# Optimization experiments

Hardware: AMD Instinct MI355X
Metric: run time of the kernel (lower is better)

The kernel has to match this reference:

```python
import jax, jax.numpy as jnp
import numpy as np

B, N, E = 4096, 64, 256      # graph pairs, nodes per drug, directed edges per drug
F, H, FP = 128, 64, 2048     # node feat dim, hidden dim, fingerprint dim


def setup_inputs() -> dict:
    key = jax.random.key(0)
    ks = jax.random.split(key, 14)
    return {
        "x1": jax.random.normal(ks[0], (B, N, F), jnp.float32),
        "x2": jax.random.normal(ks[1], (B, N, F), jnp.float32),
        "edge1": jax.random.randint(ks[2], (B, 2, E), 0, N, jnp.int32),
        "edge2": jax.random.randint(ks[3], (B, 2, E), 0, N, jnp.int32),
        "fp1": jax.random.uniform(ks[4], (B, FP), jnp.float32),
        "fp2": jax.random.uniform(ks[5], (B, FP), jnp.float32),
        "W1": jax.random.normal(ks[6], (F, H), jnp.float32) * 0.05,
        "b1": jnp.zeros((H,), jnp.float32),
        "W2": jax.random.normal(ks[7], (H, H), jnp.float32) * 0.05,
        "b2": jnp.zeros((H,), jnp.float32),
        "Wm1": jax.random.normal(ks[8], (2 * H + 2 * FP, 256), jnp.float32) * 0.02,
        "bm1": jnp.zeros((256,), jnp.float32),
        "Wm2": jax.random.normal(ks[9], (256, 1), jnp.float32) * 0.05,
        "bm2": jnp.zeros((1,), jnp.float32),
    }


def gcn_conv(x, src, dst, W, b):
    """PyG GCNConv: self-loops + symmetric normalization, aggregated at dst."""
    n = x.shape[0]
    loops = jnp.arange(n, dtype=src.dtype)
    s = jnp.concatenate([src, loops])
    d = jnp.concatenate([dst, loops])
    deg = jax.ops.segment_sum(jnp.ones_like(d, jnp.float32), d, num_segments=n)
    norm = jax.lax.rsqrt(deg)                      # deg >= 1 due to self-loops
    xw = x @ W                                     # [n, H]
    msg = xw[s] * (norm[s] * norm[d])[:, None]     # [n+E, H]
    return jax.ops.segment_sum(msg, d, num_segments=n) + b


def encode(x, edges, W1, b1, W2, b2):
    src, dst = edges[0], edges[1]
    h = jax.nn.relu(gcn_conv(x, src, dst, W1, b1))
    h = jax.nn.relu(gcn_conv(h, src, dst, W2, b2))
    return h.mean(axis=0)                          # global_mean_pool (1 graph)


_encode_b = jax.vmap(encode, in_axes=(0, 0, None, None, None, None))


def reference(x1, x2, edge1, edge2, fp1, fp2, W1, b1, W2, b2, Wm1, bm1, Wm2, bm2):
    h1 = _encode_b(x1, edge1, W1, b1, W2, b2)      # [B, H]
    h2 = _encode_b(x2, edge2, W1, b1, W2, b2)      # [B, H]
    fused = jnp.concatenate([h1, h2, fp1, fp2], axis=1)  # [B, 2H+2FP]
    hidden = jax.nn.relu(fused @ Wm1 + bm1)
    return jax.nn.sigmoid(hidden @ Wm2 + bm2).reshape(-1)
```

## Files before the change

### kernel.cpp

```cpp
#include <hip/hip_runtime.h>
#include <math.h>

#define B_PAIRS 4096
#define NNODES  64
#define NEDGES  256
#define FDIM    128
#define HDIM    64
#define FPDIM   2048
#define MDIM    256
#define KTOT    4224
#define SLICE   8704

typedef __attribute__((ext_vector_type(4))) float f32x4;
typedef __bf16 bf16x8 __attribute__((ext_vector_type(8)));

__device__ __forceinline__ unsigned short f2bf(float f) {
    return __builtin_bit_cast(unsigned short, (__bf16)f);
}
__device__ __forceinline__ unsigned pack2(float a, float b) {
    return (unsigned)f2bf(a) | ((unsigned)f2bf(b) << 16);
}
__device__ __forceinline__ unsigned long long pack4(float a, float b, float c, float d) {
    return (unsigned long long)pack2(a, b) | ((unsigned long long)pack2(c, d) << 32);
}

__global__ void prep_weights(const float* __restrict__ W1, const float* __restrict__ W2,
                             unsigned short* __restrict__ W1t, unsigned short* __restrict__ W2t) {
    const int t0 = blockIdx.x * 256 + threadIdx.x;
    const int stride = gridDim.x * 256;
    for (int i = t0; i < HDIM * FDIM; i += stride) {
        const int n = i >> 7, k = i & 127;
        W1t[i] = f2bf(W1[k * HDIM + n]);
    }
    for (int i = t0; i < HDIM * HDIM; i += stride) {
        const int n = i >> 6, k = i & 63;
        W2t[i] = f2bf(W2[k * HDIM + n]);
    }
}

__global__ __launch_bounds__(256)
void prep_wm1(const float* __restrict__ Wm1, unsigned short* __restrict__ Wm1t) {
    __shared__ float tile[32][33];
    const int k0 = blockIdx.x * 32, n0 = blockIdx.y * 32;
    const int t = threadIdx.x;
    const int c = t & 31, r8 = t >> 5;
    #pragma unroll
    for (int rr = r8; rr < 32; rr += 8)
        tile[rr][c] = Wm1[(size_t)(k0 + rr) * MDIM + n0 + c];
    __syncthreads();
    #pragma unroll
    for (int j = 0; j < 4; ++j) {
        const int n = n0 + r8 + 8 * j;
        Wm1t[(size_t)n * KTOT + k0 + c] = f2bf(tile[c][r8 + 8 * j]);
    }
}

#define WAITLDS() do { __asm__ volatile("s_waitcnt lgkmcnt(0)" ::: "memory"); \
                       __builtin_amdgcn_sched_barrier(0); } while (0)

__global__ __launch_bounds__(256, 2)
void encode_kernel(const float* __restrict__ x1, const float* __restrict__ x2,
                   const int* __restrict__ e1, const int* __restrict__ e2,
                   const unsigned short* __restrict__ W1t, const float* __restrict__ b1,
                   const unsigned short* __restrict__ W2t, const float* __restrict__ b2,
                   float* __restrict__ hbuf) {
    __shared__ __align__(16) unsigned char lds[4 * SLICE];
    const int wid = threadIdx.x >> 6;
    const int t   = threadIdx.x & 63;
    const int gid  = blockIdx.x * 4 + wid;
    const int drug = gid >> 12;
    const int b    = gid & (B_PAIRS - 1);
    const float* x  = (drug ? x2 : x1) + (size_t)b * NNODES * FDIM;
    const int*   eg = (drug ? e2 : e1) + (size_t)b * 2 * NEDGES;

    const int lr = t & 15, lg = t >> 4;
    const unsigned swl = (unsigned)(lr & 7) << 4;

    unsigned char* sl = lds + wid * SLICE;
    unsigned* cnt = (unsigned*)sl;
    float*    nrm = (float*)(sl + 8448);

    float4 xalo[16];
    #pragma unroll
    for (int mt = 0; mt < 2; ++mt) {
        const float* xr = x + (size_t)(16 * mt + lr) * FDIM + 8 * lg;
        #pragma unroll
        for (int ks = 0; ks < 4; ++ks) {
            xalo[mt * 8 + 2 * ks]     = ((const float4*)(xr + 32 * ks))[0];
            xalo[mt * 8 + 2 * ks + 1] = ((const float4*)(xr + 32 * ks))[1];
        }
    }
    const int4 s4 = ((const int4*)eg)[t];
    const int4 d4 = ((const int4*)eg)[t + 64];

    #pragma unroll
    for (int i = 0; i < 8; ++i) ((uint4*)cnt)[t + 64 * i] = make_uint4(0, 0, 0, 0);
    cnt[2048 + t] = 0;
    WAITLDS();

    {
        const int ss[4] = {s4.x, s4.y, s4.z, s4.w};
        const int dd[4] = {d4.x, d4.y, d4.z, d4.w};
        #pragma unroll
        for (int i = 0; i < 4; ++i)
            atomicAdd(&cnt[dd[i] * 33 + (ss[i] >> 1)], 1u << ((ss[i] & 1) * 16));
    }
    WAITLDS();

    float4 xahi[16];
    #pragma unroll
    for (int mt = 0; mt < 2; ++mt) {
        const float* xr2 = x + (size_t)(16 * (mt + 2) + lr) * FDIM + 8 * lg;
        #pragma unroll
        for (int ks = 0; ks < 4; ++ks) {
            xahi[mt * 8 + 2 * ks]     = ((const float4*)(xr2 + 32 * ks))[0];
            xahi[mt * 8 + 2 * ks + 1] = ((const float4*)(xr2 + 32 * ks))[1];
        }
    }

    {
        unsigned ssum = 0;
        #pragma unroll
        for (int j = 0; j < 33; ++j) {
            const unsigned w = cnt[t * 33 + j];
            ssum += (w & 0xffffu) + (w >> 16);
        }
        nrm[t] = rsqrtf((float)ssum + 1.0f);
    }
    WAITLDS();

    bf16x8 bw1[16];
    #pragma unroll
    for (int nt = 0; nt < 4; ++nt)
        #pragma unroll
        for (int ks = 0; ks < 4; ++ks)
            bw1[nt * 4 + ks] = *(const bf16x8*)(W1t + (16 * nt + lr) * FDIM + 32 * ks + 8 * lg);

    bf16x8 ahat[8];
    {
        const float ncol[2][8] = {
            { nrm[8 * lg + 0], nrm[8 * lg + 1], nrm[8 * lg + 2], nrm[8 * lg + 3],
              nrm[8 * lg + 4], nrm[8 * lg + 5], nrm[8 * lg + 6], nrm[8 * lg + 7] },
            { nrm[32 + 8 * lg + 0], nrm[32 + 8 * lg + 1], nrm[32 + 8 * lg + 2], nrm[32 + 8 * lg + 3],
              nrm[32 + 8 * lg + 4], nrm[32 + 8 * lg + 5], nrm[32 + 8 * lg + 6], nrm[32 + 8 * lg + 7] }
        };
        #pragma unroll
        for (int q = 0; q < 4; ++q) {
            const int r = 16 * q + lr;
            const float nr = nrm[r];
            #pragma unroll
            for (int ks = 0; ks < 2; ++ks) {
                const int c0 = 32 * ks + 8 * lg;
                const uint4 w = *(const uint4*)(cnt + r * 33 + (c0 >> 1));
                const unsigned ww[4] = { w.x, w.y, w.z, w.w };
                bf16x8 f;
                #pragma unroll
                for (int e = 0; e < 8; ++e) {
                    const int c = c0 + e;
                    const unsigned m = (e & 1) ? (ww[e >> 1] >> 16) : (ww[e >> 1] & 0xffffu);
                    const float v = (float)(m + (r == c ? 1u : 0u)) * nr * ncol[ks][e];
                    f[e] = (__bf16)v;
                }
                ahat[q * 2 + ks] = f;
            }
        }
    }
    WAITLDS();

    #pragma unroll
    for (int half = 0; half < 2; ++half) {
        const float4* xs = half ? xahi : xalo;
        #pragma unroll
        for (int m2i = 0; m2i < 2; ++m2i) {
            const int mt = half * 2 + m2i;
            f32x4 acc[4];
            #pragma unroll
            for (int nt = 0; nt < 4; ++nt) acc[nt] = (f32x4){0.f, 0.f, 0.f, 0.f};
            #pragma unroll
            for (int ks = 0; ks < 4; ++ks) {
                bf16x8 a;
                const float4 u = xs[m2i * 8 + 2 * ks], v = xs[m2i * 8 + 2 * ks + 1];
                a[0] = (__bf16)u.x; a[1] = (__bf16)u.y; a[2] = (__bf16)u.z; a[3] = (__bf16)u.w;
                a[4] = (__bf16)v.x; a[5] = (__bf16)v.y; a[6] = (__bf16)v.z; a[7] = (__bf16)v.w;
                #pragma unroll
                for (int nt = 0; nt < 4; ++nt)
                    acc[nt] = __builtin_amdgcn_mfma_f32_16x16x32_bf16(a, bw1[nt * 4 + ks], acc[nt], 0, 0, 0);
            }
            const unsigned m2 = (unsigned)(2 * (16 * mt + 4 * lg));
            #pragma unroll
            for (int nt = 0; nt < 4; ++nt) {
                const int f = 16 * nt + lr;
                *(unsigned long long*)(sl + (unsigned)f * 128 + (m2 ^ swl)) =
                    pack4(acc[nt][0], acc[nt][1], acc[nt][2], acc[nt][3]);
            }
        }
    }
    WAITLDS();

    {
        bf16x8 ta[8];
        #pragma unroll
        for (int mt = 0; mt < 4; ++mt)
            #pragma unroll
            for (int ks = 0; ks < 2; ++ks)
                ta[mt * 2 + ks] = *(const bf16x8*)(sl + (unsigned)(16 * mt + lr) * 128 +
                                                   (((unsigned)(64 * ks + 16 * lg)) ^ swl));
        WAITLDS();
        #pragma unroll
        for (int mt = 0; mt < 4; ++mt) {
            f32x4 acc[4];
            #pragma unroll
            for (int nt = 0; nt < 4; ++nt) acc[nt] = (f32x4){0.f, 0.f, 0.f, 0.f};
            #pragma unroll
            for (int ks = 0; ks < 2; ++ks)
                #pragma unroll
                for (int nt = 0; nt < 4; ++nt)
                    acc[nt] = __builtin_amdgcn_mfma_f32_16x16x32_bf16(ta[mt * 2 + ks], ahat[nt * 2 + ks], acc[nt], 0, 0, 0);
            const int m0 = 16 * mt + 4 * lg;
            const float4 b1v = *(const float4*)(b1 + m0);
            const unsigned m2 = (unsigned)(2 * m0);
            #pragma unroll
            for (int nt = 0; nt < 4; ++nt) {
                const int d = 16 * nt + lr;
                const float v0 = fmaxf(acc[nt][0] + b1v.x, 0.f);
                const float v1 = fmaxf(acc[nt][1] + b1v.y, 0.f);
                const float v2 = fmaxf(acc[nt][2] + b1v.z, 0.f);
                const float v3 = fmaxf(acc[nt][3] + b1v.w, 0.f);
                *(unsigned long long*)(sl + (unsigned)d * 128 + (m2 ^ swl)) =
                    pack4(v0, v1, v2, v3);
            }
        }
    }
    WAITLDS();

    {
        bf16x8 ta[8], bw2[8];
        #pragma unroll
        for (int mt = 0; mt < 4; ++mt)
            #pragma unroll
            for (int ks = 0; ks < 2; ++ks)
                ta[mt * 2 + ks] = *(const bf16x8*)(sl + (unsigned)(16 * mt + lr) * 128 +
                                                   (((unsigned)(64 * ks + 16 * lg)) ^ swl));
        #pragma unroll
        for (int nt = 0; nt < 4; ++nt)
            #pragma unroll
            for (int ks = 0; ks < 2; ++ks)
                bw2[nt * 2 + ks] = *(const bf16x8*)(W2t + (16 * nt + lr) * HDIM + 32 * ks + 8 * lg);
        WAITLDS();
        #pragma unroll
        for (int mt = 0; mt < 4; ++mt) {
            f32x4 acc[4];
            #pragma unroll
            for (int nt = 0; nt < 4; ++nt) acc[nt] = (f32x4){0.f, 0.f, 0.f, 0.f};
            #pragma unroll
            for (int ks = 0; ks < 2; ++ks)
                #pragma unroll
                for (int nt = 0; nt < 4; ++nt)
                    acc[nt] = __builtin_amdgcn_mfma_f32_16x16x32_bf16(ta[mt * 2 + ks], bw2[nt * 2 + ks], acc[nt], 0, 0, 0);
            const unsigned m2 = (unsigned)(2 * (16 * mt + 4 * lg));
            #pragma unroll
            for (int nt = 0; nt < 4; ++nt) {
                const int n = 16 * nt + lr;
                *(unsigned long long*)(sl + (unsigned)n * 128 + (m2 ^ swl)) =
                    pack4(acc[nt][0], acc[nt][1], acc[nt][2], acc[nt][3]);
            }
        }
    }
    WAITLDS();

    {
        bf16x8 bt3[8];
        #pragma unroll
        for (int nt = 0; nt < 4; ++nt)
            #pragma unroll
            for (int ks = 0; ks < 2; ++ks)
                bt3[nt * 2 + ks] = *(const bf16x8*)(sl + (unsigned)(16 * nt + lr) * 128 +
                                                    (((unsigned)(64 * ks + 16 * lg)) ^ swl));
        float b2v[4], p[4];
        #pragma unroll
        for (int nt = 0; nt < 4; ++nt) { b2v[nt] = b2[16 * nt + lr]; p[nt] = 0.f; }
        #pragma unroll
        for (int mt = 0; mt < 4; ++mt) {
            f32x4 acc[4];
            #pragma unroll
            for (int nt = 0; nt < 4; ++nt) acc[nt] = (f32x4){0.f, 0.f, 0.f, 0.f};
            #pragma unroll
            for (int ks = 0; ks < 2; ++ks)
                #pragma unroll
                for (int nt = 0; nt < 4; ++nt)
                    acc[nt] = __builtin_amdgcn_mfma_f32_16x16x32_bf16(ahat[mt * 2 + ks], bt3[nt * 2 + ks], acc[nt], 0, 0, 0);
            #pragma unroll
            for (int nt = 0; nt < 4; ++nt) {
                #pragma unroll
                for (int j = 0; j < 4; ++j) p[nt] += fmaxf(acc[nt][j] + b2v[nt], 0.f);
            }
        }
        #pragma unroll
        for (int nt = 0; nt < 4; ++nt) {
            p[nt] += __shfl_xor(p[nt], 16, 64);
            p[nt] += __shfl_xor(p[nt], 32, 64);
        }
        if (lg == 0) {
            float* hout = hbuf + ((size_t)drug * B_PAIRS + b) * HDIM;
            #pragma unroll
            for (int nt = 0; nt < 4; ++nt) hout[16 * nt + lr] = p[nt] * (1.0f / 64.0f);
        }
    }
}

__global__ __launch_bounds__(256)
void fused_mlp_kernel(const float* __restrict__ fp1, const float* __restrict__ fp2,
                      const float* __restrict__ hbuf,
                      const unsigned short* __restrict__ Wm1t,
                      const float* __restrict__ bm1, const float* __restrict__ Wm2,
                      const float* __restrict__ bm2, float* __restrict__ out) {
    __shared__ __align__(16) unsigned char lds[8448];
    float* pool = (float*)(lds + 8192);
    const int t = threadIdx.x;
    const int lane = t & 63, wid = t >> 6;
    const int lr = lane & 15, lg = lane >> 4;
    const int pair0 = blockIdx.x * 16;

    const int r  = t >> 4;
    const int kc = (t & 15) << 3;
    const int pr = pair0 + r;
    const unsigned wOff = (unsigned)r * 256 + (((unsigned)(2 * kc)) ^ ((unsigned)(r & 7) << 4));

    f32x4 acc[4];
    #pragma unroll
    for (int nf = 0; nf < 4; ++nf) acc[nf] = (f32x4){0.f, 0.f, 0.f, 0.f};

    const unsigned short* brow[4];
    #pragma unroll
    for (int nf = 0; nf < 4; ++nf)
        brow[nf] = Wm1t + (size_t)(64 * wid + 16 * nf + lr) * KTOT + 8 * lg;

    float4 va, vb;
    #define LOAD_A(s)                                                                  \
        {                                                                              \
            const float* src;                                                          \
            if ((s) == 0)                                                              \
                src = (kc < 64) ? hbuf + (size_t)pr * HDIM + kc                        \
                                : hbuf + (size_t)(B_PAIRS + pr) * HDIM + (kc - 64);    \
            else if ((s) <= 16)                                                        \
                src = fp1 + (size_t)pr * FPDIM + ((s) - 1) * 128 + kc;                 \
            else                                                                       \
                src = fp2 + (size_t)pr * FPDIM + ((s) - 17) * 128 + kc;                \
            va = ((const float4*)src)[0];                                              \
            vb = ((const float4*)src)[1];                                              \
        }
    #define STORE_A(base)                                                              \
        *(uint4*)((base) + wOff) = make_uint4(pack2(va.x, va.y), pack2(va.z, va.w),    \
                                              pack2(vb.x, vb.y), pack2(vb.z, vb.w));

    LOAD_A(0);
    STORE_A(lds);
    for (int s = 0; s < 33; ++s) {
        const bool more = (s + 1 < 33);
        if (more) LOAD_A(s + 1);
        __syncthreads();
        const unsigned char* buf = lds + (unsigned)((s & 1) << 12);
        const unsigned asw = (unsigned)(lr & 7) << 4;
        const int kglob = s << 7;
        #pragma unroll
        for (int ks = 0; ks < 4; ++ks) {
            const unsigned kb = (unsigned)(64 * ks + 16 * lg);
            const bf16x8 a = *(const bf16x8*)(buf + (unsigned)lr * 256 + (kb ^ asw));
            #pragma unroll
            for (int nf = 0; nf < 4; ++nf) {
                const bf16x8 bw = *(const bf16x8*)(brow[nf] + kglob + 32 * ks);
                acc[nf] = __builtin_amdgcn_mfma_f32_16x16x32_bf16(a, bw, acc[nf], 0, 0, 0);
            }
        }
        if (more) STORE_A(lds + (unsigned)(((s + 1) & 1) << 12));
    }

    float bm1v[4], wm2v[4];
    #pragma unroll
    for (int nf = 0; nf < 4; ++nf) {
        const int n = 64 * wid + 16 * nf + lr;
        bm1v[nf] = bm1[n];
        wm2v[nf] = Wm2[n];
    }
    #pragma unroll
    for (int reg = 0; reg < 4; ++reg) {
        float p = 0.f;
        #pragma unroll
        for (int nf = 0; nf < 4; ++nf)
            p += fmaxf(acc[nf][reg] + bm1v[nf], 0.f) * wm2v[nf];
        p += __shfl_xor(p, 1, 64);
        p += __shfl_xor(p, 2, 64);
        p += __shfl_xor(p, 4, 64);
        p += __shfl_xor(p, 8, 64);
        if (lr == 0) pool[wid * 16 + 4 * lg + reg] = p;
    }
    __syncthreads();
    if (t < 16) {
        const float y = pool[t] + pool[16 + t] + pool[32 + t] + pool[48 + t] + bm2[0];
        out[pair0 + t] = 1.0f / (1.0f + expf(-y));
    }
    #undef LOAD_A
    #undef STORE_A
}

extern "C" void kernel_launch(void* const* d_in, const int* in_sizes, int n_in,
                              void* d_out, int out_size, void* d_ws, size_t ws_size,
                              hipStream_t stream) {
    const float* x1  = (const float*)d_in[0];
    const float* x2  = (const float*)d_in[1];
    const int*   e1  = (const int*)d_in[2];
    const int*   e2  = (const int*)d_in[3];
    const float* fp1 = (const float*)d_in[4];
    const float* fp2 = (const float*)d_in[5];
    const float* W1  = (const float*)d_in[6];
    const float* b1  = (const float*)d_in[7];
    const float* W2  = (const float*)d_in[8];
    const float* b2  = (const float*)d_in[9];
    const float* Wm1 = (const float*)d_in[10];
    const float* bm1 = (const float*)d_in[11];
    const float* Wm2 = (const float*)d_in[12];
    const float* bm2 = (const float*)d_in[13];
    float* out  = (float*)d_out;

    float* hbuf = (float*)d_ws;
    unsigned short* W1t  = (unsigned short*)((char*)d_ws + (2 << 20));
    unsigned short* W2t  = W1t + HDIM * FDIM;
    unsigned short* Wm1t = (unsigned short*)((char*)d_ws + (3 << 20));

    hipLaunchKernelGGL(prep_weights, dim3(16), dim3(256), 0, stream, W1, W2, W1t, W2t);
    hipLaunchKernelGGL(prep_wm1, dim3(132, 8), dim3(256), 0, stream, Wm1, Wm1t);
    hipLaunchKernelGGL(encode_kernel, dim3(2 * B_PAIRS / 4), dim3(256), 0, stream,
                       x1, x2, e1, e2, W1t, b1, W2t, b2, hbuf);
    hipLaunchKernelGGL(fused_mlp_kernel, dim3(B_PAIRS / 16), dim3(256), 0, stream,
                       fp1, fp2, hbuf, Wm1t, bm1, Wm2, bm2, out);
}
```

Measured before the change: 165.8 us.

## Overlap fingerprint MLP GEMM with graph encoding in a combined kernel

Splits the first MLP layer so the large fingerprint part (K=4096) runs as extra blocks interleaved with the GCN encoder blocks in one launch, writing partial sums to a workspace buffer G. A small final kernel then adds the hidden-feature part (K=128), applies bias, ReLU, the second layer and sigmoid. The goal is to overlap the bandwidth-heavy fingerprint reads with the encoder work and avoid serialising the two phases. The cost is an extra fp32 round trip through global memory for G, plus the fingerprint blocks sharing the encoder's large LDS allocation and its launch bounds, which can limit occupancy.

After: 219.8 us. 1.33x slower.

```diff
diff --git a/kernel.cpp b/kernel.cpp
--- a/kernel.cpp
+++ b/kernel.cpp
@@ -23,6 +23,12 @@
 __device__ __forceinline__ unsigned long long pack4(float a, float b, float c, float d) {
     return (unsigned long long)pack2(a, b) | ((unsigned long long)pack2(c, d) << 32);
 }
+__device__ __forceinline__ bf16x8 cvt8(float4 u, float4 v) {
+    bf16x8 a;
+    a[0] = (__bf16)u.x; a[1] = (__bf16)u.y; a[2] = (__bf16)u.z; a[3] = (__bf16)u.w;
+    a[4] = (__bf16)v.x; a[5] = (__bf16)v.y; a[6] = (__bf16)v.z; a[7] = (__bf16)v.w;
+    return a;
+}
 
 __global__ void prep_weights(const float* __restrict__ W1, const float* __restrict__ W2,
                              unsigned short* __restrict__ W1t, unsigned short* __restrict__ W2t) {
@@ -59,15 +65,85 @@
                        __builtin_amdgcn_sched_barrier(0); } while (0)
 
 __global__ __launch_bounds__(256, 2)
-void encode_kernel(const float* __restrict__ x1, const float* __restrict__ x2,
-                   const int* __restrict__ e1, const int* __restrict__ e2,
-                   const unsigned short* __restrict__ W1t, const float* __restrict__ b1,
-                   const unsigned short* __restrict__ W2t, const float* __restrict__ b2,
-                   float* __restrict__ hbuf) {
+void mega_kernel(const float* __restrict__ x1, const float* __restrict__ x2,
+                 const int* __restrict__ e1, const int* __restrict__ e2,
+                 const unsigned short* __restrict__ W1t, const float* __restrict__ b1,
+                 const unsigned short* __restrict__ W2t, const float* __restrict__ b2,
+                 float* __restrict__ hbuf,
+                 const float* __restrict__ fp1, const float* __restrict__ fp2,
+                 const unsigned short* __restrict__ Wm1t, float* __restrict__ G) {
     __shared__ __align__(16) unsigned char lds[4 * SLICE];
-    const int wid = threadIdx.x >> 6;
-    const int t   = threadIdx.x & 63;
-    const int gid  = blockIdx.x * 4 + wid;
+    const int bid = blockIdx.x;
+    const int q = bid / 9, rr9 = bid % 9;
+    const int t256 = threadIdx.x;
+
+    if (rr9 == 8) {
+        const int lane = t256 & 63, wid = t256 >> 6;
+        const int lr = lane & 15, lg = lane >> 4;
+        const int pair0 = q * 16;
+        const int srow = t256 >> 4;
+        const int kc = (t256 & 15) << 3;
+        const int pr = pair0 + srow;
+        const unsigned wOff = (unsigned)srow * 256 +
+                              (((unsigned)(2 * kc)) ^ ((unsigned)(srow & 7) << 4));
+
+        f32x4 acc[4];
+        #pragma unroll
+        for (int nf = 0; nf < 4; ++nf) acc[nf] = (f32x4){0.f, 0.f, 0.f, 0.f};
+
+        const unsigned short* brow[4];
+        #pragma unroll
+        for (int nf = 0; nf < 4; ++nf)
+            brow[nf] = Wm1t + (size_t)(64 * wid + 16 * nf + lr) * KTOT + 8 * lg;
+
+        float4 va, vb;
+        #define LOAD_A(s)                                                              \
+            {                                                                          \
+                const float* src = ((s) <= 16)                                         \
+                    ? fp1 + (size_t)pr * FPDIM + ((s) - 1) * 128 + kc                  \
+                    : fp2 + (size_t)pr * FPDIM + ((s) - 17) * 128 + kc;                \
+                va = ((const float4*)src)[0];                                          \
+                vb = ((const float4*)src)[1];                                          \
+            }
+        #define STORE_A(base)                                                          \
+            *(uint4*)((base) + wOff) = make_uint4(pack2(va.x, va.y), pack2(va.z, va.w),\
+                                                  pack2(vb.x, vb.y), pack2(vb.z, vb.w));
+
+        LOAD_A(1);
+        STORE_A(lds + 4096);
+        for (int s = 1; s <= 32; ++s) {
+            const bool more = (s < 32);
+            if (more) LOAD_A(s + 1);
+            __syncthreads();
+            const unsigned char* buf = lds + (unsigned)((s & 1) << 12);
+            const unsigned asw = (unsigned)(lr & 7) << 4;
+            const int kglob = s << 7;
+            #pragma unroll
+            for (int ks = 0; ks < 4; ++ks) {
+                const unsigned kb = (unsigned)(64 * ks + 16 * lg);
+                const bf16x8 a = *(const bf16x8*)(buf + (unsigned)lr * 256 + (kb ^ asw));
+                #pragma unroll
+                for (int nf = 0; nf < 4; ++nf) {
+                    const bf16x8 bw = *(const bf16x8*)(brow[nf] + kglob + 32 * ks);
+                    acc[nf] = __builtin_amdgcn_mfma_f32_16x16x32_bf16(a, bw, acc[nf], 0, 0, 0);
+                }
+            }
+            if (more) STORE_A(lds + (unsigned)(((s + 1) & 1) << 12));
+        }
+        #undef LOAD_A
+        #undef STORE_A
+
+        #pragma unroll
+        for (int nf = 0; nf < 4; ++nf)
+            #pragma unroll
+            for (int reg = 0; reg < 4; ++reg)
+                G[(size_t)(pair0 + 4 * lg + reg) * MDIM + 64 * wid + 16 * nf + lr] = acc[nf][reg];
+        return;
+    }
+
+    const int wid = t256 >> 6;
+    const int t   = t256 & 63;
+    const int gid  = (q * 8 + rr9) * 4 + wid;
     const int drug = gid >> 12;
     const int b    = gid & (B_PAIRS - 1);
     const float* x  = (drug ? x2 : x1) + (size_t)b * NNODES * FDIM;
@@ -145,8 +221,8 @@
               nrm[32 + 8 * lg + 4], nrm[32 + 8 * lg + 5], nrm[32 + 8 * lg + 6], nrm[32 + 8 * lg + 7] }
         };
         #pragma unroll
-        for (int q = 0; q < 4; ++q) {
-            const int r = 16 * q + lr;
+        for (int qq = 0; qq < 4; ++qq) {
+            const int r = 16 * qq + lr;
             const float nr = nrm[r];
             #pragma unroll
             for (int ks = 0; ks < 2; ++ks) {
@@ -161,7 +237,7 @@
                     const float v = (float)(m + (r == c ? 1u : 0u)) * nr * ncol[ks][e];
                     f[e] = (__bf16)v;
                 }
-                ahat[q * 2 + ks] = f;
+                ahat[qq * 2 + ks] = f;
             }
         }
     }
@@ -178,10 +254,7 @@
             for (int nt = 0; nt < 4; ++nt) acc[nt] = (f32x4){0.f, 0.f, 0.f, 0.f};
             #pragma unroll
             for (int ks = 0; ks < 4; ++ks) {
-                bf16x8 a;
-                const float4 u = xs[m2i * 8 + 2 * ks], v = xs[m2i * 8 + 2 * ks + 1];
-                a[0] = (__bf16)u.x; a[1] = (__bf16)u.y; a[2] = (__bf16)u.z; a[3] = (__bf16)u.w;
-                a[4] = (__bf16)v.x; a[5] = (__bf16)v.y; a[6] = (__bf16)v.z; a[7] = (__bf16)v.w;
+                const bf16x8 a = cvt8(xs[m2i * 8 + 2 * ks], xs[m2i * 8 + 2 * ks + 1]);
                 #pragma unroll
                 for (int nt = 0; nt < 4; ++nt)
                     acc[nt] = __builtin_amdgcn_mfma_f32_16x16x32_bf16(a, bw1[nt * 4 + ks], acc[nt], 0, 0, 0);
@@ -309,70 +382,36 @@
 }
 
 __global__ __launch_bounds__(256)
-void fused_mlp_kernel(const float* __restrict__ fp1, const float* __restrict__ fp2,
-                      const float* __restrict__ hbuf,
-                      const unsigned short* __restrict__ Wm1t,
-                      const float* __restrict__ bm1, const float* __restrict__ Wm2,
-                      const float* __restrict__ bm2, float* __restrict__ out) {
-    __shared__ __align__(16) unsigned char lds[8448];
-    float* pool = (float*)(lds + 8192);
+void fuse_final(const float* __restrict__ hbuf, const float* __restrict__ G,
+                const unsigned short* __restrict__ Wm1t,
+                const float* __restrict__ bm1, const float* __restrict__ Wm2,
+                const float* __restrict__ bm2, float* __restrict__ out) {
+    __shared__ float pool[64];
     const int t = threadIdx.x;
     const int lane = t & 63, wid = t >> 6;
     const int lr = lane & 15, lg = lane >> 4;
     const int pair0 = blockIdx.x * 16;
 
-    const int r  = t >> 4;
-    const int kc = (t & 15) << 3;
-    const int pr = pair0 + r;
-    const unsigned wOff = (unsigned)r * 256 + (((unsigned)(2 * kc)) ^ ((unsigned)(r & 7) << 4));
-
     f32x4 acc[4];
     #pragma unroll
-    for (int nf = 0; nf < 4; ++nf) acc[nf] = (f32x4){0.f, 0.f, 0.f, 0.f};
-
-    const unsigned short* brow[4];
-    #pragma unroll
     for (int nf = 0; nf < 4; ++nf)
-        brow[nf] = Wm1t + (size_t)(64 * wid + 16 * nf + lr) * KTOT + 8 * lg;
-
-    float4 va, vb;
-    #define LOAD_A(s)                                                                  \
-        {                                                                              \
-            const float* src;                                                          \
-            if ((s) == 0)                                                              \
-                src = (kc < 64) ? hbuf + (size_t)pr * HDIM + kc                        \
-                                : hbuf + (size_t)(B_PAIRS + pr) * HDIM + (kc - 64);    \
-            else if ((s) <= 16)                                                        \
-                src = fp1 + (size_t)pr * FPDIM + ((s) - 1) * 128 + kc;                 \
-            else                                                                       \
-                src = fp2 + (size_t)pr * FPDIM + ((s) - 17) * 128 + kc;                \
-            va = ((const float4*)src)[0];                                              \
-            vb = ((const float4*)src)[1];                                              \
-        }
-    #define STORE_A(base)                                                              \
-        *(uint4*)((base) + wOff) = make_uint4(pack2(va.x, va.y), pack2(va.z, va.w),    \
-                                              pack2(vb.x, vb.y), pack2(vb.z, vb.w));
-
-    LOAD_A(0);
-    STORE_A(lds);
-    for (int s = 0; s < 33; ++s) {
-        const bool more = (s + 1 < 33);
-        if (more) LOAD_A(s + 1);
-        __syncthreads();
-        const unsigned char* buf = lds + (unsigned)((s & 1) << 12);
-        const unsigned asw = (unsigned)(lr & 7) << 4;
-        const int kglob = s << 7;
-        #pragma unroll
-        for (int ks = 0; ks < 4; ++ks) {
-            const unsigned kb = (unsigned)(64 * ks + 16 * lg);
-            const bf16x8 a = *(const bf16x8*)(buf + (unsigned)lr * 256 + (kb ^ asw));
-            #pragma unroll
-            for (int nf = 0; nf < 4; ++nf) {
-                const bf16x8 bw = *(const bf16x8*)(brow[nf] + kglob + 32 * ks);
-                acc[nf] = __builtin_amdgcn_mfma_f32_16x16x32_bf16(a, bw, acc[nf], 0, 0, 0);
-            }
-        }
-        if (more) STORE_A(lds + (unsigned)(((s + 1) & 1) << 12));
+        #pragma unroll
+        for (int reg = 0; reg < 4; ++reg)
+            acc[nf][reg] = G[(size_t)(pair0 + 4 * lg + reg) * MDIM + 64 * wid + 16 * nf + lr];
+
+    #pragma unroll
+    for (int ks = 0; ks < 4; ++ks) {
+        const float* hsrc = (ks < 2)
+            ? hbuf + (size_t)(pair0 + lr) * HDIM + 32 * ks + 8 * lg
+            : hbuf + (size_t)(B_PAIRS + pair0 + lr) * HDIM + 32 * (ks - 2) + 8 * lg;
+        const float4 u = ((const float4*)hsrc)[0];
+        const float4 v = ((const float4*)hsrc)[1];
+        const bf16x8 a = cvt8(u, v);
+        #pragma unroll
+        for (int nf = 0; nf < 4; ++nf) {
+            const bf16x8 bw = *(const bf16x8*)(Wm1t + (size_t)(64 * wid + 16 * nf + lr) * KTOT + 32 * ks + 8 * lg);
+            acc[nf] = __builtin_amdgcn_mfma_f32_16x16x32_bf16(a, bw, acc[nf], 0, 0, 0);
+        }
     }
 
     float bm1v[4], wm2v[4];
@@ -399,8 +438,6 @@
         const float y = pool[t] + pool[16 + t] + pool[32 + t] + pool[48 + t] + bm2[0];
         out[pair0 + t] = 1.0f / (1.0f + expf(-y));
     }
-    #undef LOAD_A
-    #undef STORE_A
 }
 
 extern "C" void kernel_launch(void* const* d_in, const int* in_sizes, int n_in,
@@ -426,11 +463,12 @@
     unsigned short* W1t  = (unsigned short*)((char*)d_ws + (2 << 20));
     unsigned short* W2t  = W1t + HDIM * FDIM;
     unsigned short* Wm1t = (unsigned short*)((char*)d_ws + (3 << 20));
+    float* G = (float*)((char*)d_ws + (6 << 20));
 
     hipLaunchKernelGGL(prep_weights, dim3(16), dim3(256), 0, stream, W1, W2, W1t, W2t);
     hipLaunchKernelGGL(prep_wm1, dim3(132, 8), dim3(256), 0, stream, Wm1, Wm1t);
-    hipLaunchKernelGGL(encode_kernel, dim3(2 * B_PAIRS / 4), dim3(256), 0, stream,
-                       x1, x2, e1, e2, W1t, b1, W2t, b2, hbuf);
-    hipLaunchKernelGGL(fused_mlp_kernel, dim3(B_PAIRS / 16), dim3(256), 0, stream,
-                       fp1, fp2, hbuf, Wm1t, bm1, Wm2, bm2, out);
-}
+    hipLaunchKernelGGL(mega_kernel, dim3(2304), dim3(256), 0, stream,
+                       x1, x2, e1, e2, W1t, b1, W2t, b2, hbuf, fp1, fp2, Wm1t, G);
+    hipLaunchKernelGGL(fuse_final, dim3(256), dim3(256), 0, stream,
+                       hbuf, G, Wm1t, bm1, Wm2, bm2, out);
+}
```

## Stream x row tiles and W1 fragments per iteration to cut register pressure

Applied to the files above, without the earlier changes.

Instead of preloading all 64 rows of x (32 float4 per lane) and all 16 W1 fragments into registers up front, the first GEMM now keeps one 16-row tile of x in registers and prefetches the next tile inside a non-unrolled loop. W1 fragments are reloaded in two passes of 8 per tile. The aim is to lower VGPR usage so more waves fit per CU and to overlap the next tile's load with the current MFMAs. In exchange, the early latency hiding from loading x before the edge-count phase is lost, and W1 is re-read from cache four times.

Result: no change. 163.2 us (-1.5%).

```diff
diff --git a/kernel.cpp b/kernel.cpp
--- a/kernel.cpp
+++ b/kernel.cpp
@@ -22,6 +22,12 @@
 }
 __device__ __forceinline__ unsigned long long pack4(float a, float b, float c, float d) {
     return (unsigned long long)pack2(a, b) | ((unsigned long long)pack2(c, d) << 32);
+}
+__device__ __forceinline__ bf16x8 cvt8(float4 u, float4 v) {
+    bf16x8 a;
+    a[0] = (__bf16)u.x; a[1] = (__bf16)u.y; a[2] = (__bf16)u.z; a[3] = (__bf16)u.w;
+    a[4] = (__bf16)v.x; a[5] = (__bf16)v.y; a[6] = (__bf16)v.z; a[7] = (__bf16)v.w;
+    return a;
 }
 
 __global__ void prep_weights(const float* __restrict__ W1, const float* __restrict__ W2,
@@ -80,14 +86,13 @@
     unsigned* cnt = (unsigned*)sl;
     float*    nrm = (float*)(sl + 8448);
 
-    float4 xalo[16];
-    #pragma unroll
-    for (int mt = 0; mt < 2; ++mt) {
-        const float* xr = x + (size_t)(16 * mt + lr) * FDIM + 8 * lg;
+    float4 xq[8];
+    {
+        const float* xr = x + (size_t)lr * FDIM + 8 * lg;
         #pragma unroll
         for (int ks = 0; ks < 4; ++ks) {
-            xalo[mt * 8 + 2 * ks]     = ((const float4*)(xr + 32 * ks))[0];
-            xalo[mt * 8 + 2 * ks + 1] = ((const float4*)(xr + 32 * ks))[1];
+            xq[2 * ks]     = ((const float4*)(xr + 32 * ks))[0];
+            xq[2 * ks + 1] = ((const float4*)(xr + 32 * ks))[1];
         }
     }
     const int4 s4 = ((const int4*)eg)[t];
@@ -106,17 +111,6 @@
             atomicAdd(&cnt[dd[i] * 33 + (ss[i] >> 1)], 1u << ((ss[i] & 1) * 16));
     }
     WAITLDS();
-
-    float4 xahi[16];
-    #pragma unroll
-    for (int mt = 0; mt < 2; ++mt) {
-        const float* xr2 = x + (size_t)(16 * (mt + 2) + lr) * FDIM + 8 * lg;
-        #pragma unroll
-        for (int ks = 0; ks < 4; ++ks) {
-            xahi[mt * 8 + 2 * ks]     = ((const float4*)(xr2 + 32 * ks))[0];
-            xahi[mt * 8 + 2 * ks + 1] = ((const float4*)(xr2 + 32 * ks))[1];
-        }
-    }
 
     {
         unsigned ssum = 0;
@@ -128,13 +122,6 @@
         nrm[t] = rsqrtf((float)ssum + 1.0f);
     }
     WAITLDS();
-
-    bf16x8 bw1[16];
-    #pragma unroll
-    for (int nt = 0; nt < 4; ++nt)
-        #pragma unroll
-        for (int ks = 0; ks < 4; ++ks)
-            bw1[nt * 4 + ks] = *(const bf16x8*)(W1t + (16 * nt + lr) * FDIM + 32 * ks + 8 * lg);
 
     bf16x8 ahat[8];
     {
@@ -167,32 +154,42 @@
     }
     WAITLDS();
 
-    #pragma unroll
-    for (int half = 0; half < 2; ++half) {
-        const float4* xs = half ? xahi : xalo;
-        #pragma unroll
-        for (int m2i = 0; m2i < 2; ++m2i) {
-            const int mt = half * 2 + m2i;
-            f32x4 acc[4];
-            #pragma unroll
-            for (int nt = 0; nt < 4; ++nt) acc[nt] = (f32x4){0.f, 0.f, 0.f, 0.f};
+    #pragma unroll 1
+    for (int q = 0; q < 4; ++q) {
+        bf16x8 af[4];
+        #pragma unroll
+        for (int ks = 0; ks < 4; ++ks) af[ks] = cvt8(xq[2 * ks], xq[2 * ks + 1]);
+        if (q < 3) {
+            const float* xr = x + (size_t)(16 * (q + 1) + lr) * FDIM + 8 * lg;
             #pragma unroll
             for (int ks = 0; ks < 4; ++ks) {
-                bf16x8 a;
-                const float4 u = xs[m2i * 8 + 2 * ks], v = xs[m2i * 8 + 2 * ks + 1];
-                a[0] = (__bf16)u.x; a[1] = (__bf16)u.y; a[2] = (__bf16)u.z; a[3] = (__bf16)u.w;
-                a[4] = (__bf16)v.x; a[5] = (__bf16)v.y; a[6] = (__bf16)v.z; a[7] = (__bf16)v.w;
-                #pragma unroll
-                for (int nt = 0; nt < 4; ++nt)
-                    acc[nt] = __builtin_amdgcn_mfma_f32_16x16x32_bf16(a, bw1[nt * 4 + ks], acc[nt], 0, 0, 0);
-            }
-            const unsigned m2 = (unsigned)(2 * (16 * mt + 4 * lg));
-            #pragma unroll
-            for (int nt = 0; nt < 4; ++nt) {
-                const int f = 16 * nt + lr;
-                *(unsigned long long*)(sl + (unsigned)f * 128 + (m2 ^ swl)) =
-                    pack4(acc[nt][0], acc[nt][1], acc[nt][2], acc[nt][3]);
-            }
+                xq[2 * ks]     = ((const float4*)(xr + 32 * ks))[0];
+                xq[2 * ks + 1] = ((const float4*)(xr + 32 * ks))[1];
+            }
+        }
+        f32x4 acc[4];
+        #pragma unroll
+        for (int nt = 0; nt < 4; ++nt) acc[nt] = (f32x4){0.f, 0.f, 0.f, 0.f};
+        #pragma unroll
+        for (int pass = 0; pass < 2; ++pass) {
+            bf16x8 bw[8];
+            #pragma unroll
+            for (int j = 0; j < 2; ++j)
+                #pragma unroll
+                for (int ks = 0; ks < 4; ++ks)
+                    bw[j * 4 + ks] = *(const bf16x8*)(W1t + (16 * (2 * pass + j) + lr) * FDIM + 32 * ks + 8 * lg);
+            #pragma unroll
+            for (int ks = 0; ks < 4; ++ks)
+                #pragma unroll
+                for (int j = 0; j < 2; ++j)
+                    acc[2 * pass + j] = __builtin_amdgcn_mfma_f32_16x16x32_bf16(af[ks], bw[j * 4 + ks], acc[2 * pass + j], 0, 0, 0);
+        }
+        const unsigned m2 = (unsigned)(2 * (16 * q + 4 * lg));
+        #pragma unroll
+        for (int nt = 0; nt < 4; ++nt) {
+            const int f = 16 * nt + lr;
+            *(unsigned long long*)(sl + (unsigned)f * 128 + (m2 ^ swl)) =
+                pack4(acc[nt][0], acc[nt][1], acc[nt][2], acc[nt][3]);
         }
     }
     WAITLDS();
```
